# Performance work log

Measured on AMD Instinct MI355X. Metric: run time of the kernel, lower is better.

The kernel has to match this reference:

```python
import jax, jax.numpy as jnp
import numpy as np

TOKENS, INPUT, HIDDEN, K = 8192, 1024, 16384, 32

def setup_inputs() -> dict:
    key = jax.random.key(0)
    ks = jax.random.split(key, 6)
    return {
        "x": jax.random.normal(ks[0], (TOKENS, INPUT), dtype=jnp.float32),
        "pre_encode_b": jax.random.normal(ks[1], (INPUT,), dtype=jnp.float32) * 0.1,
        "W": jax.random.normal(ks[2], (HIDDEN, INPUT), dtype=jnp.float32) * 0.01,
        "WT": jax.random.normal(ks[3], (INPUT, HIDDEN), dtype=jnp.float32) * 0.01,
        "b1": jax.random.normal(ks[4], (HIDDEN,), dtype=jnp.float32) * 0.1,
        "b2": jax.random.normal(ks[5], (INPUT,), dtype=jnp.float32) * 0.1,
        "k": K,
    }

def reference(x, pre_encode_b, W, WT, b1, b2, k):
    # encode: dense GEMM [token, hidden]
    xc = x - pre_encode_b
    preacts = jnp.matmul(xc, WT) + b1
    # topk over hidden dim
    vals, idx = jax.lax.top_k(preacts, k)          # [token, k]
    # decode: gather rows of W by topk indices, weighted sum
    Wg = W[idx]                                    # [token, k, input]
    x_hat = jnp.einsum('tk,tki->ti', vals, Wg) + b2
    return x_hat
```

## Files before the change

kernel.cpp:

```cpp
#include <hip/hip_runtime.h>
#include <hip/hip_fp16.h>

#define TOKENS 8192
#define INPUT  1024
#define HIDDEN 16384
#define KSEL   32
#define CANDCAP 96
#define TWO_E  0.006f

typedef __attribute__((ext_vector_type(8))) short bf16x8;
typedef __attribute__((ext_vector_type(4))) float f32x4;

#define GLOAD_LDS16(g, l) __builtin_amdgcn_global_load_lds(              \
    (const __attribute__((address_space(1))) void*)(const void*)(g),     \
    (__attribute__((address_space(3))) void*)(void*)(l), 16, 0, 0)

__device__ inline short f2bf(float f) {
    unsigned u = __float_as_uint(f);
    u += 0x7FFFu + ((u >> 16) & 1u);
    return (short)(u >> 16);
}

__device__ inline float keyToF(unsigned k) {
    unsigned o = (k & 0x8000u) ? (k ^ 0x8000u) : (~k & 0xFFFFu);
    return __half2float(__ushort_as_half((unsigned short)o));
}

__global__ __launch_bounds__(256) void conv_x(
    const float* __restrict__ x, const float* __restrict__ peb,
    short* __restrict__ Abf)
{
    const int g = (blockIdx.x * 256 + threadIdx.x) * 8;
    const int col = g & (INPUT - 1);
    float4 v0 = *(const float4*)&x[g];
    float4 v1 = *(const float4*)&x[g + 4];
    float4 p0 = *(const float4*)&peb[col];
    float4 p1 = *(const float4*)&peb[col + 4];
    short o[8] = {f2bf(v0.x - p0.x), f2bf(v0.y - p0.y), f2bf(v0.z - p0.z), f2bf(v0.w - p0.w),
                  f2bf(v1.x - p1.x), f2bf(v1.y - p1.y), f2bf(v1.z - p1.z), f2bf(v1.w - p1.w)};
    *(bf16x8*)&Abf[g] = *(bf16x8*)o;
}

__global__ __launch_bounds__(256) void transp2(
    const float* __restrict__ WT, float* __restrict__ WTT, short* __restrict__ Btb)
{
    __shared__ float tl[64][65];
    const int bx = blockIdx.x, by = blockIdx.y;
    const int tid = threadIdx.x;
    const int r0 = tid >> 6, c = tid & 63;
#pragma unroll
    for (int i = 0; i < 16; ++i) {
        int r = i * 4 + r0;
        tl[r][c] = WT[(size_t)(by * 64 + r) * HIDDEN + bx * 64 + c];
    }
    __syncthreads();
#pragma unroll
    for (int i = 0; i < 16; ++i) {
        int a = i * 4 + r0;
        float v = tl[c][a];
        size_t o = (size_t)(bx * 64 + a) * INPUT + by * 64 + c;
        WTT[o] = v;
        Btb[o] = f2bf(v);
    }
}

__global__ __launch_bounds__(256) void conv_whf(
    const float* __restrict__ W, unsigned short* __restrict__ Whf)
{
    const size_t g = ((size_t)blockIdx.x * 256 + threadIdx.x) * 8;
    float4 v0 = *(const float4*)&W[g];
    float4 v1 = *(const float4*)&W[g + 4];
    unsigned short o[8] = {
        __half_as_ushort(__float2half(v0.x)), __half_as_ushort(__float2half(v0.y)),
        __half_as_ushort(__float2half(v0.z)), __half_as_ushort(__float2half(v0.w)),
        __half_as_ushort(__float2half(v1.x)), __half_as_ushort(__float2half(v1.y)),
        __half_as_ushort(__float2half(v1.z)), __half_as_ushort(__float2half(v1.w))};
    *(uint4*)&Whf[g] = *(uint4*)o;
}

__global__ __launch_bounds__(512, 2) void gemm_bf16_256(
    const short* __restrict__ A,
    const short* __restrict__ Bt,
    const float* __restrict__ bias1,
    unsigned short* __restrict__ pre16,
    int tok0)
{
    __shared__ short lds[65536];
    const char* L = (const char*)lds;
    const int tid = threadIdx.x;
    const int lane = tid & 63;
    const int w = tid >> 6;
    const int wr = w >> 2, wc = w & 3;

    const int nbx = gridDim.x;
    const int My  = gridDim.y;
    int flat = blockIdx.y * nbx + blockIdx.x;
    const int xcd = flat & 7;
    const int idx = flat >> 3;
    const int colsPerX = nbx >> 3;
    const int q = idx / My;
    const int bm = idx - q * My;
    const int bn = xcd * colsPerX + q;

    const int row0 = tok0 + bm * 256;
    const int col0 = bn * 256;

    const int xr = (lane & 7) << 4;
    const int koff = (lane >> 4) * 16;
    const int swk0 = koff ^ xr;
    const int swk1 = (64 + koff) ^ xr;
    const int aA0 = (wr * 128 + (lane & 15)) * 128 + swk0;
    const int aA1 = (wr * 128 + (lane & 15)) * 128 + swk1;
    const int aB0 = (wc * 64 + (lane & 15)) * 128 + swk0;
    const int aB1 = (wc * 64 + (lane & 15)) * 128 + swk1;

    const int srd = tid >> 3;
    const int scol = ((tid & 7) * 16) ^ ((srd & 7) << 4);
    const short* Asrc = A  + (size_t)(row0 + srd) * INPUT + (scol >> 1);
    const short* Bsrc = Bt + (size_t)(col0 + srd) * INPUT + (scol >> 1);

    f32x4 acc[8][4];
#pragma unroll
    for (int m = 0; m < 8; ++m)
#pragma unroll
        for (int n = 0; n < 4; ++n) acc[m][n] = (f32x4){0.f, 0.f, 0.f, 0.f};

    auto stageA = [&](int slot, int half, int kt) {
        const size_t so = (size_t)(half * 128) * INPUT + kt * 64;
        short* dst = lds + slot * 32768 + half * 8192 + tid * 8;
        GLOAD_LDS16(Asrc + so, dst);
        GLOAD_LDS16(Asrc + so + (size_t)64 * INPUT, dst + 4096);
    };
    auto stageB = [&](int slot, int half, int kt) {
        const size_t so = (size_t)(half * 128) * INPUT + kt * 64;
        short* dst = lds + slot * 32768 + 16384 + half * 8192 + tid * 8;
        GLOAD_LDS16(Bsrc + so, dst);
        GLOAD_LDS16(Bsrc + so + (size_t)64 * INPUT, dst + 4096);
    };

    bf16x8 AQ[8], BL[4], BH[4];

#define RD_A(SAb, mfbase)                                                       \
    _Pragma("unroll") for (int mf = 0; mf < 4; ++mf) {                          \
        AQ[mf * 2 + 0] = *(const bf16x8*)(L + (SAb) + aA0 + ((mfbase) + mf) * 2048); \
        AQ[mf * 2 + 1] = *(const bf16x8*)(L + (SAb) + aA1 + ((mfbase) + mf) * 2048); \
    }
#define RD_B(SBb, BF, nfbase)                                                   \
    _Pragma("unroll") for (int nf = 0; nf < 2; ++nf) {                          \
        BF[nf * 2 + 0] = *(const bf16x8*)(L + (SBb) + aB0 + ((nfbase) + nf) * 2048); \
        BF[nf * 2 + 1] = *(const bf16x8*)(L + (SBb) + aB1 + ((nfbase) + nf) * 2048); \
    }
#define MFMA_Q(BF, mb, nb)                                                      \
    __builtin_amdgcn_s_setprio(1);                                              \
    _Pragma("unroll") for (int mf = 0; mf < 4; ++mf)                            \
        _Pragma("unroll") for (int nf = 0; nf < 2; ++nf)                        \
            _Pragma("unroll") for (int kk = 0; kk < 2; ++kk)                    \
                acc[(mb) + mf][(nb) + nf] = __builtin_amdgcn_mfma_f32_16x16x32_bf16( \
                    AQ[mf * 2 + kk], BF[nf * 2 + kk], acc[(mb) + mf][(nb) + nf], 0, 0, 0); \
    __builtin_amdgcn_s_setprio(0);
#define BAR()  __builtin_amdgcn_s_barrier()
#define LGKM0() asm volatile("s_waitcnt lgkmcnt(0)" ::: "memory")

    stageA(0, 0, 0); stageA(0, 1, 0);
    stageB(0, 0, 0); stageB(0, 1, 0);
    stageB(1, 0, 1); stageB(1, 1, 1);
    asm volatile("s_waitcnt vmcnt(4)" ::: "memory");
    BAR();

    for (int i = 0; i < 8; ++i) {
        const int kt1 = 2 * i + 1, kt2 = 2 * i + 2, kt3 = 2 * i + 3;
        const bool s2 = kt2 < 16, s3 = kt3 < 16;
        RD_A(0, 0); RD_B(32768, BL, 0);
        stageA(1, 0, kt1);
        BAR(); LGKM0();
        MFMA_Q(BL, 0, 0);
        BAR();
        RD_B(32768, BH, 2);
        stageA(1, 1, kt1);
        BAR(); LGKM0();
        MFMA_Q(BH, 0, 2);
        BAR();
        RD_A(0, 4);
        if (s2) stageB(0, 0, kt2);
        BAR(); LGKM0();
        MFMA_Q(BL, 4, 0);
        BAR();
        if (s2) stageB(0, 1, kt2);
        BAR(); LGKM0();
        MFMA_Q(BH, 4, 2);
        if (i < 7) { asm volatile("s_waitcnt vmcnt(4)" ::: "memory"); }
        else       { asm volatile("s_waitcnt vmcnt(0)" ::: "memory"); }
        BAR();
        RD_A(65536, 0); RD_B(98304, BL, 0);
        if (s2) stageA(0, 0, kt2);
        BAR(); LGKM0();
        MFMA_Q(BL, 0, 0);
        BAR();
        RD_B(98304, BH, 2);
        if (s2) stageA(0, 1, kt2);
        BAR(); LGKM0();
        MFMA_Q(BH, 0, 2);
        BAR();
        RD_A(65536, 4);
        if (s3) stageB(1, 0, kt3);
        BAR(); LGKM0();
        MFMA_Q(BL, 4, 0);
        BAR();
        if (s3) stageB(1, 1, kt3);
        BAR(); LGKM0();
        MFMA_Q(BH, 4, 2);
        if (i < 7) { asm volatile("s_waitcnt vmcnt(4)" ::: "memory"); }
        BAR();
    }
#undef RD_A
#undef RD_B
#undef MFMA_Q
#undef BAR
#undef LGKM0

    __syncthreads();

    float bb[4];
#pragma unroll
    for (int nf = 0; nf < 4; ++nf)
        bb[nf] = bias1[col0 + wc * 64 + nf * 16 + (lane & 15)];

    unsigned short* LE = (unsigned short*)lds;
#pragma unroll
    for (int mf = 0; mf < 8; ++mf) {
#pragma unroll
        for (int nf = 0; nf < 4; ++nf) {
#pragma unroll
            for (int r = 0; r < 4; ++r) {
                int er = wr * 16 + (lane >> 4) * 4 + r;
                int ec = wc * 64 + nf * 16 + (lane & 15);
                LE[er * 264 + ec] = __half_as_ushort(__float2half(acc[mf][nf][r] + bb[nf]));
            }
        }
        __syncthreads();
#pragma unroll
        for (int rd = 0; rd < 2; ++rd) {
            int idx2 = rd * 512 + tid;
            int er = idx2 >> 5, c8 = (idx2 & 31) * 8;
            int b = er >> 4;
            int grow = bm * 256 + b * 128 + mf * 16 + (er & 15);
            uint4 v = *(const uint4*)&LE[er * 264 + c8];
            *(uint4*)&pre16[(size_t)grow * HIDDEN + col0 + c8] = v;
        }
        __syncthreads();
    }
}

__global__ __launch_bounds__(256) void topcand3(
    const unsigned short* __restrict__ pre16,
    int* __restrict__ cand, float* __restrict__ scr,
    int* __restrict__ ncand, int tok0)
{
    const int tid = threadIdx.x;
    const int t = blockIdx.x;
    const unsigned short* row = pre16 + (size_t)t * HIDDEN;

    unsigned pk[32];
#pragma unroll
    for (int i = 0; i < 8; ++i) {
        uint4 raw = *(const uint4*)&row[(size_t)tid * 64 + i * 8];
        unsigned rr[4] = {raw.x, raw.y, raw.z, raw.w};
#pragma unroll
        for (int j = 0; j < 4; ++j) {
            unsigned lo16 = rr[j] & 0xFFFFu, hi16 = rr[j] >> 16;
            lo16 ^= (((lo16 >> 15) * 0xFFFFu) | 0x8000u);
            hi16 ^= (((hi16 >> 15) * 0xFFFFu) | 0x8000u);
            pk[i * 4 + j] = lo16 | (hi16 << 16);
        }
    }

    __shared__ unsigned wsum[4];
    const int lane = tid & 63, wid = tid >> 6;

    auto countGE = [&](unsigned tau) -> unsigned {
        unsigned c = 0;
#pragma unroll
        for (int i = 0; i < 32; ++i) {
            c += ((pk[i] & 0xFFFFu) >= tau) ? 1u : 0u;
            c += ((pk[i] >> 16) >= tau) ? 1u : 0u;
        }
#pragma unroll
        for (int s = 32; s > 0; s >>= 1) c += __shfl_xor(c, s, 64);
        if (lane == 0) wsum[wid] = c;
        __syncthreads();
        unsigned tot = wsum[0] + wsum[1] + wsum[2] + wsum[3];
        __syncthreads();
        return tot;
    };

    unsigned lo = 0, hi = 0xFFFFu;
    for (int it = 0; it < 17 && lo < hi; ++it) {
        unsigned mid = (lo + hi + 1) >> 1;
        unsigned c = countGE(mid);
        if (c >= 40u) { lo = mid; if (c <= 48u) break; }
        else hi = mid - 1;
    }
    float v40 = keyToF(lo);
    float vthr = v40 - (TWO_E + 0.002f);
    unsigned kthr = (unsigned)__half_as_ushort(__float2half(vthr));
    kthr ^= (((kthr >> 15) * 0xFFFFu) | 0x8000u);

    unsigned mycnt = 0;
#pragma unroll
    for (int i = 0; i < 32; ++i) {
        mycnt += ((pk[i] & 0xFFFFu) >= kthr) ? 1u : 0u;
        mycnt += ((pk[i] >> 16) >= kthr) ? 1u : 0u;
    }
    unsigned inc = mycnt;
#pragma unroll
    for (int s = 1; s < 64; s <<= 1) {
        unsigned o = __shfl_up(inc, s, 64);
        if (lane >= s) inc += o;
    }
    __shared__ unsigned wtot[4];
    if (lane == 63) wtot[wid] = inc;
    __syncthreads();
    unsigned base = inc - mycnt;
    for (int k = 0; k < wid; ++k) base += wtot[k];
    unsigned tot = wtot[0] + wtot[1] + wtot[2] + wtot[3];

    const int gtok = tok0 + t;
    unsigned pos = base;
#pragma unroll
    for (int i = 0; i < 32; ++i) {
        unsigned l16 = pk[i] & 0xFFFFu, h16 = pk[i] >> 16;
        if (l16 >= kthr) {
            if (pos < CANDCAP) {
                cand[(size_t)gtok * CANDCAP + pos] = tid * 64 + i * 2;
                scr[(size_t)gtok * CANDCAP + pos] = keyToF(l16);
            }
            ++pos;
        }
        if (h16 >= kthr) {
            if (pos < CANDCAP) {
                cand[(size_t)gtok * CANDCAP + pos] = tid * 64 + i * 2 + 1;
                scr[(size_t)gtok * CANDCAP + pos] = keyToF(h16);
            }
            ++pos;
        }
    }
    if (tid == 0) ncand[gtok] = (int)(tot < (unsigned)CANDCAP ? tot : (unsigned)CANDCAP);
}

__global__ __launch_bounds__(256) void rescore_select(
    const float* __restrict__ x, const float* __restrict__ peb,
    const float* __restrict__ WTT, const float* __restrict__ bias1,
    const int* __restrict__ cand, const float* __restrict__ scr,
    const int* __restrict__ ncand,
    float* __restrict__ selv, int* __restrict__ seli)
{
    const int t = blockIdx.x;
    const int tid = threadIdx.x;
    __shared__ double xcs[INPUT];
    __shared__ float sv[CANDCAP];
    __shared__ int   si[CANDCAP];
    __shared__ double bex[CANDCAP];
    __shared__ unsigned char flg[CANDCAP];
    __shared__ unsigned char self_[CANDCAP];
    __shared__ short bandlist[CANDCAP];
    __shared__ float s32s;
    __shared__ int bns, nins;

    const int nc0 = ncand[t];
    const int nc = nc0 < CANDCAP ? nc0 : CANDCAP;

#pragma unroll
    for (int i = 0; i < 4; ++i) {
        int j = tid + i * 256;
        xcs[j] = (double)x[(size_t)t * INPUT + j] - (double)peb[j];
    }
    if (tid < nc) {
        sv[tid] = scr[(size_t)t * CANDCAP + tid];
        si[tid] = cand[(size_t)t * CANDCAP + tid];
    }
    __syncthreads();

    if (tid < nc) {
        float v = sv[tid]; int h = si[tid];
        int r = 0;
        for (int k = 0; k < nc; ++k) {
            float vk = sv[k];
            if (vk > v || (vk == v && si[k] < h)) ++r;
        }
        if (r == 31) s32s = v;
    }
    __syncthreads();
    const float s32 = s32s;

    if (tid < nc) {
        float v = sv[tid];
        flg[tid] = (v > s32 + TWO_E) ? 2 : ((v >= s32 - TWO_E) ? 1 : 0);
    }
    __syncthreads();
    if (tid == 0) {
        int bn = 0, nin = 0;
        for (int k = 0; k < nc; ++k) {
            if (flg[k] == 1) bandlist[bn++] = (short)k;
            else if (flg[k] == 2) ++nin;
        }
        bns = bn; nins = nin;
    }
    __syncthreads();
    const int bn = bns, need = KSEL - nins;

    const int wid = tid >> 6, lane = tid & 63;
    for (int j0 = wid * 2; j0 < bn; j0 += 8) {
        const int j1 = j0 + 1;
        const int c0 = bandlist[j0];
        const int c1 = (j1 < bn) ? bandlist[j1] : c0;
        const int h0 = si[c0], h1 = si[c1];
        const float* w0 = WTT + (size_t)h0 * INPUT;
        const float* w1 = WTT + (size_t)h1 * INPUT;
        double s0 = 0.0, s1 = 0.0;
#pragma unroll
        for (int st = 0; st < 16; ++st) {
            const double xv = xcs[lane + st * 64];
            s0 += (double)w0[lane + st * 64] * xv;
            s1 += (double)w1[lane + st * 64] * xv;
        }
#pragma unroll
        for (int off = 32; off > 0; off >>= 1) {
            s0 += __shfl_xor(s0, off, 64);
            s1 += __shfl_xor(s1, off, 64);
        }
        if (lane == 0) {
            bex[c0] = s0 + (double)bias1[h0];
            if (j1 < bn) bex[c1] = s1 + (double)bias1[h1];
        }
    }
    __syncthreads();

    if (tid < nc) {
        int s = 0;
        if (flg[tid] == 2) s = 1;
        else if (flg[tid] == 1) {
            double v = bex[tid]; int h = si[tid];
            int r = 0;
            for (int k = 0; k < bn; ++k) {
                int ck = bandlist[k];
                double vk = bex[ck];
                if (vk > v || (vk == v && si[ck] < h)) ++r;
            }
            if (r < need) s = 1;
        }
        self_[tid] = (unsigned char)s;
    }
    __syncthreads();
    if (tid < nc && self_[tid]) {
        int pos = 0;
        for (int k = 0; k < tid; ++k) pos += self_[k];
        if (pos < KSEL) {
            selv[(size_t)t * KSEL + pos] = (flg[tid] == 2) ? sv[tid] : (float)bex[tid];
            seli[(size_t)t * KSEL + pos] = si[tid];
        }
    }
}

__global__ __launch_bounds__(512) void decode512(
    const float* __restrict__ selv, const int* __restrict__ seli,
    const unsigned short* __restrict__ Whf, const float* __restrict__ b2,
    float* __restrict__ out)
{
    const int t = blockIdx.x;
    const int tid = threadIdx.x;
    const int jh = tid >> 8;
    const int cpos = tid & 255;
    const int c = cpos * 4;
    __shared__ float sv[KSEL];
    __shared__ int si[KSEL];
    __shared__ float4 red[256];
    if (tid < KSEL) {
        sv[tid] = selv[(size_t)t * KSEL + tid];
        si[tid] = seli[(size_t)t * KSEL + tid];
    }
    __syncthreads();
    float4 acc = {0.f, 0.f, 0.f, 0.f};
    const int j0 = jh * 16;
#pragma unroll 8
    for (int j = j0; j < j0 + 16; ++j) {
        uint2 raw = *(const uint2*)&Whf[(size_t)si[j] * INPUT + c];
        const float s = sv[j];
        float2 f0 = __half22float2(*(__half2*)&raw.x);
        float2 f1 = __half22float2(*(__half2*)&raw.y);
        acc.x += s * f0.x; acc.y += s * f0.y; acc.z += s * f1.x; acc.w += s * f1.y;
    }
    if (jh == 1) red[cpos] = acc;
    __syncthreads();
    if (jh == 0) {
        float4 o = red[cpos];
        float4 bb = *(const float4*)&b2[c];
        o.x += acc.x + bb.x; o.y += acc.y + bb.y;
        o.z += acc.z + bb.z; o.w += acc.w + bb.w;
        *(float4*)&out[(size_t)t * INPUT + c] = o;
    }
}

extern "C" void kernel_launch(void* const* d_in, const int* in_sizes, int n_in,
                              void* d_out, int out_size, void* d_ws, size_t ws_size,
                              hipStream_t stream) {
    const float* x   = (const float*)d_in[0];
    const float* peb = (const float*)d_in[1];
    const float* W   = (const float*)d_in[2];
    const float* WT  = (const float*)d_in[3];
    const float* b1  = (const float*)d_in[4];
    const float* b2  = (const float*)d_in[5];
    float* out = (float*)d_out;

    char* p = (char*)d_ws;
    int*   candb = (int*)p;            p += (size_t)TOKENS * CANDCAP * 4;
    float* scrb  = (float*)p;          p += (size_t)TOKENS * CANDCAP * 4;
    int*   ncb   = (int*)p;            p += (size_t)TOKENS * 4;
    float* selvb = (float*)p;          p += (size_t)TOKENS * KSEL * 4;
    int*   selib = (int*)p;            p += (size_t)TOKENS * KSEL * 4;
    float* WTT   = (float*)p;          p += (size_t)HIDDEN * INPUT * 4;
    short* Abf   = (short*)p;          p += (size_t)TOKENS * INPUT * 2;
    short* Btb   = (short*)p;          p += (size_t)HIDDEN * INPUT * 2;
    unsigned short* Whf = (unsigned short*)p; p += (size_t)HIDDEN * INPUT * 2;
    unsigned short* pre16 = (unsigned short*)p;

    size_t used = (size_t)(p - (char*)d_ws);
    size_t avail = ws_size > used ? ws_size - used : 0;
    long cap = (long)(avail / ((size_t)HIDDEN * 2));
    cap = (cap / 256) * 256;
    if (cap > 2048) cap = 2048;
    if (cap < 256) cap = 256;

    conv_x<<<dim3(TOKENS * INPUT / (256 * 8)), dim3(256), 0, stream>>>(x, peb, Abf);
    transp2<<<dim3(HIDDEN / 64, INPUT / 64), dim3(256), 0, stream>>>(WT, WTT, Btb);
    conv_whf<<<dim3((unsigned)((size_t)HIDDEN * INPUT / (256 * 8))), dim3(256), 0, stream>>>(W, Whf);

    for (int tok0 = 0; tok0 < TOKENS; tok0 += (int)cap) {
        int M = TOKENS - tok0;
        if (M > cap) M = (int)cap;
        gemm_bf16_256<<<dim3(HIDDEN / 256, M / 256), dim3(512), 0, stream>>>(
            Abf, Btb, b1, pre16, tok0);
        topcand3<<<dim3(M), dim3(256), 0, stream>>>(pre16, candb, scrb, ncb, tok0);
    }

    rescore_select<<<dim3(TOKENS), dim3(256), 0, stream>>>(
        x, peb, WTT, b1, candb, scrb, ncb, selvb, selib);
    decode512<<<dim3(TOKENS), dim3(512), 0, stream>>>(selvb, selib, Whf, b2, out);
}
```

Baseline: 698.3 us.

## Rescore and select top-k with one wavefront per token instead of a block

The rescore/select stage now maps one token per 64-lane wavefront, with four tokens per block, in place of one 256-thread block per token. Ranking, band classification, compaction and output positions are computed with shuffles, ballots and popcounts rather than shared memory and block-wide barriers. The centered input row is held in registers. This removes barriers, serial single-thread loops and idle threads, at the cost of serial per-wave band rescoring that may lose latency hiding when the band is large.

```diff
diff --git a/kernel.cpp b/kernel.cpp
--- a/kernel.cpp
+++ b/kernel.cpp
@@ -347,116 +347,108 @@
     if (tid == 0) ncand[gtok] = (int)(tot < (unsigned)CANDCAP ? tot : (unsigned)CANDCAP);
 }
 
-__global__ __launch_bounds__(256) void rescore_select(
+__global__ __launch_bounds__(256) void rescore_select_wave(
     const float* __restrict__ x, const float* __restrict__ peb,
     const float* __restrict__ WTT, const float* __restrict__ bias1,
     const int* __restrict__ cand, const float* __restrict__ scr,
     const int* __restrict__ ncand,
     float* __restrict__ selv, int* __restrict__ seli)
 {
-    const int t = blockIdx.x;
-    const int tid = threadIdx.x;
-    __shared__ double xcs[INPUT];
-    __shared__ float sv[CANDCAP];
-    __shared__ int   si[CANDCAP];
-    __shared__ double bex[CANDCAP];
-    __shared__ unsigned char flg[CANDCAP];
-    __shared__ unsigned char self_[CANDCAP];
-    __shared__ short bandlist[CANDCAP];
-    __shared__ float s32s;
-    __shared__ int bns, nins;
+    const int wid = threadIdx.x >> 6, lane = threadIdx.x & 63;
+    const int t = blockIdx.x * 4 + wid;
+
+    __shared__ double bexL[4][CANDCAP];
+    __shared__ short bandL[4][CANDCAP];
+
+    double xc[16];
+#pragma unroll
+    for (int st = 0; st < 16; ++st) {
+        int j = lane + st * 64;
+        xc[st] = (double)x[(size_t)t * INPUT + j] - (double)peb[j];
+    }
 
     const int nc0 = ncand[t];
     const int nc = nc0 < CANDCAP ? nc0 : CANDCAP;
 
-#pragma unroll
-    for (int i = 0; i < 4; ++i) {
-        int j = tid + i * 256;
-        xcs[j] = (double)x[(size_t)t * INPUT + j] - (double)peb[j];
-    }
-    if (tid < nc) {
-        sv[tid] = scr[(size_t)t * CANDCAP + tid];
-        si[tid] = cand[(size_t)t * CANDCAP + tid];
-    }
-    __syncthreads();
-
-    if (tid < nc) {
-        float v = sv[tid]; int h = si[tid];
-        int r = 0;
-        for (int k = 0; k < nc; ++k) {
-            float vk = sv[k];
-            if (vk > v || (vk == v && si[k] < h)) ++r;
-        }
-        if (r == 31) s32s = v;
-    }
-    __syncthreads();
-    const float s32 = s32s;
-
-    if (tid < nc) {
-        float v = sv[tid];
-        flg[tid] = (v > s32 + TWO_E) ? 2 : ((v >= s32 - TWO_E) ? 1 : 0);
-    }
-    __syncthreads();
-    if (tid == 0) {
-        int bn = 0, nin = 0;
-        for (int k = 0; k < nc; ++k) {
-            if (flg[k] == 1) bandlist[bn++] = (short)k;
-            else if (flg[k] == 2) ++nin;
-        }
-        bns = bn; nins = nin;
-    }
-    __syncthreads();
-    const int bn = bns, need = KSEL - nins;
-
-    const int wid = tid >> 6, lane = tid & 63;
-    for (int j0 = wid * 2; j0 < bn; j0 += 8) {
-        const int j1 = j0 + 1;
-        const int c0 = bandlist[j0];
-        const int c1 = (j1 < bn) ? bandlist[j1] : c0;
-        const int h0 = si[c0], h1 = si[c1];
-        const float* w0 = WTT + (size_t)h0 * INPUT;
-        const float* w1 = WTT + (size_t)h1 * INPUT;
-        double s0 = 0.0, s1 = 0.0;
-#pragma unroll
-        for (int st = 0; st < 16; ++st) {
-            const double xv = xcs[lane + st * 64];
-            s0 += (double)w0[lane + st * 64] * xv;
-            s1 += (double)w1[lane + st * 64] * xv;
-        }
-#pragma unroll
-        for (int off = 32; off > 0; off >>= 1) {
-            s0 += __shfl_xor(s0, off, 64);
-            s1 += __shfl_xor(s1, off, 64);
-        }
-        if (lane == 0) {
-            bex[c0] = s0 + (double)bias1[h0];
-            if (j1 < bn) bex[c1] = s1 + (double)bias1[h1];
-        }
-    }
-    __syncthreads();
-
-    if (tid < nc) {
-        int s = 0;
-        if (flg[tid] == 2) s = 1;
-        else if (flg[tid] == 1) {
-            double v = bex[tid]; int h = si[tid];
-            int r = 0;
-            for (int k = 0; k < bn; ++k) {
-                int ck = bandlist[k];
-                double vk = bex[ck];
-                if (vk > v || (vk == v && si[ck] < h)) ++r;
+    float sv0 = 0.f, sv1 = 0.f;
+    int si0 = 0, si1 = 0;
+    const bool a0 = lane < nc, a1 = (64 + lane) < nc;
+    if (a0) { sv0 = scr[(size_t)t * CANDCAP + lane]; si0 = cand[(size_t)t * CANDCAP + lane]; }
+    if (a1) { sv1 = scr[(size_t)t * CANDCAP + 64 + lane]; si1 = cand[(size_t)t * CANDCAP + 64 + lane]; }
+
+    int r0 = 0, r1 = 0;
+    for (int k = 0; k < nc; ++k) {
+        float vk; int hk;
+        if (k < 64) { vk = __shfl(sv0, k, 64); hk = __shfl(si0, k, 64); }
+        else        { vk = __shfl(sv1, k - 64, 64); hk = __shfl(si1, k - 64, 64); }
+        if (a0 && (vk > sv0 || (vk == sv0 && hk < si0))) ++r0;
+        if (a1 && (vk > sv1 || (vk == sv1 && hk < si1))) ++r1;
+    }
+
+    unsigned long long b31_0 = __ballot(a0 && r0 == 31);
+    unsigned long long b31_1 = __ballot(a1 && r1 == 31);
+    float s32;
+    if (b31_0) s32 = __shfl(sv0, (int)__ffsll((long long)b31_0) - 1, 64);
+    else       s32 = __shfl(sv1, (int)__ffsll((long long)b31_1) - 1, 64);
+
+    const int f0 = a0 ? ((sv0 > s32 + TWO_E) ? 2 : ((sv0 >= s32 - TWO_E) ? 1 : 0)) : 0;
+    const int f1 = a1 ? ((sv1 > s32 + TWO_E) ? 2 : ((sv1 >= s32 - TWO_E) ? 1 : 0)) : 0;
+
+    const unsigned long long mi0 = __ballot(f0 == 2), mi1 = __ballot(f1 == 2);
+    const unsigned long long mb0 = __ballot(f0 == 1), mb1 = __ballot(f1 == 1);
+    const int nin = __popcll(mi0) + __popcll(mi1);
+    const int bn = __popcll(mb0) + __popcll(mb1);
+    const int need = KSEL - nin;
+
+    const unsigned long long ltmask = (lane == 63) ? 0x7FFFFFFFFFFFFFFFull
+                                                   : ((1ull << lane) - 1ull);
+    if (f0 == 1) bandL[wid][__popcll(mb0 & ltmask)] = (short)lane;
+    if (f1 == 1) bandL[wid][__popcll(mb0) + __popcll(mb1 & ltmask)] = (short)(64 + lane);
+
+    for (int jb = 0; jb < bn; ++jb) {
+        const int c = bandL[wid][jb];
+        const int h = (c < 64) ? __shfl(si0, c, 64) : __shfl(si1, c - 64, 64);
+        const float* wrow = WTT + (size_t)h * INPUT;
+        double s = 0.0;
+#pragma unroll
+        for (int st = 0; st < 16; ++st)
+            s += (double)wrow[lane + st * 64] * xc[st];
+#pragma unroll
+        for (int off = 32; off > 0; off >>= 1)
+            s += __shfl_xor(s, off, 64);
+        if (lane == 0) bexL[wid][c] = s + (double)bias1[h];
+    }
+
+    int s0 = 0, s1 = 0;
+    {
+        double v0 = 0.0, v1 = 0.0;
+        if (f0 == 1) v0 = bexL[wid][lane];
+        if (f1 == 1) v1 = bexL[wid][64 + lane];
+        int rb0 = 0, rb1 = 0;
+        for (int k = 0; k < bn; ++k) {
+            const int ck = bandL[wid][k];
+            const int hk = (ck < 64) ? __shfl(si0, ck, 64) : __shfl(si1, ck - 64, 64);
+            const double vk = bexL[wid][ck];
+            if (f0 == 1 && (vk > v0 || (vk == v0 && hk < si0))) ++rb0;
+            if (f1 == 1 && (vk > v1 || (vk == v1 && hk < si1))) ++rb1;
+        }
+        if (f0 == 2 || (f0 == 1 && rb0 < need)) s0 = 1;
+        if (f1 == 2 || (f1 == 1 && rb1 < need)) s1 = 1;
+
+        const unsigned long long ms0 = __ballot(s0), ms1 = __ballot(s1);
+        if (s0) {
+            int pos = __popcll(ms0 & ltmask);
+            if (pos < KSEL) {
+                selv[(size_t)t * KSEL + pos] = (f0 == 2) ? sv0 : (float)v0;
+                seli[(size_t)t * KSEL + pos] = si0;
             }
-            if (r < need) s = 1;
-        }
-        self_[tid] = (unsigned char)s;
-    }
-    __syncthreads();
-    if (tid < nc && self_[tid]) {
-        int pos = 0;
-        for (int k = 0; k < tid; ++k) pos += self_[k];
-        if (pos < KSEL) {
-            selv[(size_t)t * KSEL + pos] = (flg[tid] == 2) ? sv[tid] : (float)bex[tid];
-            seli[(size_t)t * KSEL + pos] = si[tid];
+        }
+        if (s1) {
+            int pos = __popcll(ms0) + __popcll(ms1 & ltmask);
+            if (pos < KSEL) {
+                selv[(size_t)t * KSEL + pos] = (f1 == 2) ? sv1 : (float)v1;
+                seli[(size_t)t * KSEL + pos] = si1;
+            }
         }
     }
 }
@@ -542,7 +534,7 @@
         topcand3<<<dim3(M), dim3(256), 0, stream>>>(pre16, candb, scrb, ncb, tok0);
     }
 
-    rescore_select<<<dim3(TOKENS), dim3(256), 0, stream>>>(
+    rescore_select_wave<<<dim3(TOKENS / 4), dim3(256), 0, stream>>>(
         x, peb, WTT, b1, candb, scrb, ncb, selvb, selib);
     decode512<<<dim3(TOKENS), dim3(512), 0, stream>>>(selvb, selib, Whf, b2, out);
 }
```

Result: faster. 618.3 us (-11.5%).
